# Kernel optimization log

Measured on AMD Instinct MI355X. Metric: run time of the kernel, lower is better.

## Reference

```python
import jax, jax.numpy as jnp
import numpy as np

N = 10000
E = 160000
IN_CH, HID, OUT = 14, 128, 4
HEADS = 8
NEG_SLOPE = 0.2


def setup_inputs() -> dict:
    key = jax.random.key(0)
    ks = jax.random.split(key, 16)
    glorot = lambda k, shape: jax.random.normal(k, shape, jnp.float32) * np.sqrt(2.0 / (shape[0] + shape[-1]))
    inp = {
        'x': jax.random.normal(ks[0], (N, IN_CH), jnp.float32),
        'edge_index': jax.random.randint(ks[1], (2, E), 0, N, jnp.int64),
        # layer 1: 14 -> 8 heads x 128, concat
        'W1': glorot(ks[2], (IN_CH, HEADS * HID)),
        'a_src1': glorot(ks[3], (HEADS, HID)),
        'a_dst1': glorot(ks[4], (HEADS, HID)),
        'b1': jnp.zeros((HEADS * HID,), jnp.float32),
        # layer 2: 1024 -> 8 heads x 128, concat
        'W2': glorot(ks[5], (HEADS * HID, HEADS * HID)),
        'a_src2': glorot(ks[6], (HEADS, HID)),
        'a_dst2': glorot(ks[7], (HEADS, HID)),
        'b2': jnp.zeros((HEADS * HID,), jnp.float32),
        # layer 3: 1024 -> 1 head x 4, mean (concat=False)
        'W3': glorot(ks[8], (HEADS * HID, OUT)),
        'a_src3': glorot(ks[9], (1, OUT)),
        'a_dst3': glorot(ks[10], (1, OUT)),
        'b3': jnp.zeros((OUT,), jnp.float32),
    }
    return inp


def gat_conv(x, src, dst, W, a_src, a_dst, b, heads, out_ch, concat):
    n = x.shape[0]
    h = (x @ W).reshape(n, heads, out_ch)                      # [N,H,C]
    al_s = jnp.sum(h * a_src, axis=-1)                         # [N,H]
    al_d = jnp.sum(h * a_dst, axis=-1)                         # [N,H]
    e = al_s[src] + al_d[dst]                                  # [E,H]
    e = jnp.where(e > 0, e, NEG_SLOPE * e)                     # LeakyReLU(0.2)
    # segment softmax over incoming edges of each dst node
    m = jax.ops.segment_max(e, dst, num_segments=n)
    ex = jnp.exp(e - m[dst])
    z = jax.ops.segment_sum(ex, dst, num_segments=n)
    alpha = ex / (z[dst] + 1e-16)                              # [E,H]
    out = jax.ops.segment_sum(h[src] * alpha[:, :, None], dst, num_segments=n)  # [N,H,C]
    out = out.reshape(n, heads * out_ch) if concat else out.mean(axis=1)
    return out + b


def reference(x, edge_index, W1, a_src1, a_dst1, b1, W2, a_src2, a_dst2, b2, W3, a_src3, a_dst3, b3):
    n = x.shape[0]
    # add self-loops (PyG GATConv default)
    loop = jnp.arange(n, dtype=edge_index.dtype)
    src = jnp.concatenate([edge_index[0], loop])
    dst = jnp.concatenate([edge_index[1], loop])
    # dropout layers are identity in eval mode
    h = gat_conv(x, src, dst, W1, a_src1, a_dst1, b1, HEADS, HID, True)
    h = jax.nn.relu(h)
    h = gat_conv(h, src, dst, W2, a_src2, a_dst2, b2, HEADS, HID, True)
    h = jax.nn.relu(h)
    h = gat_conv(h, src, dst, W3, a_src3, a_dst3, b3, 1, OUT, False)
    h = jax.nn.relu(h)
    return h
```

## Files before the change

### kernel.cpp

```cpp
#include <hip/hip_runtime.h>

typedef unsigned short ushort_t;
typedef unsigned int uint32;

#define N_NODES 10000
#define N_EDGES 160000
#define ET (N_NODES + N_EDGES)
#define MPAD 10112
#define HT 1024
#define HEADS 8
#define NEG 0.2f

#define O_FLAG     0
#define O_SRC      256
#define O_DST      (O_SRC + 680192)
#define O_COUNTS   (O_DST + 680192)
#define O_OFFS     (O_COUNTS + 40192)
#define O_CURS     (O_OFFS + 40192)
#define O_SSORT    (O_CURS + 40192)
#define O_ALS      (O_SSORT + 680192)
#define O_ALD      (O_ALS + 320000)
#define O_AL3S     (O_ALD + 320000)
#define O_AL3D     (O_AL3S + 40192)
#define O_H3       (O_AL3D + 40192)
#define O_XF       (O_H3 + 160000)
#define O_W1F      (O_XF + 560128)
#define O_AS1F     (O_W1F + 57344)
#define O_W3F      (O_AS1F + 24576)
#define O_S3F      (O_W3F + 16384)
#define O_W2T      (O_S3F + 768)
#define O_BUFA     (O_W2T + 2097152)
#define O_BUFB     (O_BUFA + 20709376)

__device__ __forceinline__ float bf2f(ushort_t u){ return __uint_as_float(((uint32)u) << 16); }
__device__ __forceinline__ ushort_t f2bf(float f){
    uint32 x = __float_as_uint(f);
    return (ushort_t)((x + 0x7fffu + ((x >> 16) & 1u)) >> 16);
}
__device__ __forceinline__ void unpack2(uint32 u, float& lo, float& hi){
    lo = __uint_as_float(u << 16);
    hi = __uint_as_float(u & 0xffff0000u);
}

typedef __bf16 bf16x8 __attribute__((ext_vector_type(8)));
typedef float  f32x4  __attribute__((ext_vector_type(4)));

typedef const __attribute__((address_space(1))) uint32* gas1_u32;
typedef       __attribute__((address_space(3))) uint32* las3_u32;

__device__ __forceinline__ void gload_lds16(const void* g, void* l){
    __builtin_amdgcn_global_load_lds((gas1_u32)g, (las3_u32)l, 16, 0, 0);
}

__device__ __forceinline__ int probe_f32(const uint32* __restrict__ w){
    int cnt = 0;
    for (int i = 0; i < 256; i++){
        uint32 e = (w[i] >> 7) & 0xffu;
        cnt += (e >= 64u && e <= 160u) ? 1 : 0;
    }
    return (cnt > 200) ? 0 : 1;
}
__device__ __forceinline__ int probe_edge64(const int* __restrict__ ei){
    int nz = 0;
    for (int i = 0; i < 128; i++) nz |= ei[2*i + 1];
    return (nz == 0) ? 1 : 0;
}

struct CvtArgs {
    const void* src[12];
    float*      dst[12];
    int         n[12];
};

__global__ __launch_bounds__(256) void k_setup(CvtArgs a, const void* __restrict__ W2,
                                               const uint32* __restrict__ w1raw,
                                               const int* __restrict__ eiraw,
                                               int* __restrict__ counts,
                                               ushort_t* __restrict__ W2T,
                                               int* __restrict__ flags){
    __shared__ ushort_t tile[32][33];
    int slice = blockIdx.y;
    int tid = threadIdx.x;
    if (slice < 12){
        int n = a.n[slice];
        int base = blockIdx.x * 1024 + tid * 4;
        if (base >= n) return;
        int f32 = probe_f32(w1raw);
        const void* s = a.src[slice];
        float* d = a.dst[slice];
        #pragma unroll
        for (int j = 0; j < 4; j++){
            int i = base + j;
            if (i < n) d[i] = f32 ? ((const float*)s)[i] : bf2f(((const ushort_t*)s)[i]);
        }
    } else if (slice == 12){
        if (blockIdx.x == 10){
            if (tid == 0) flags[0] = probe_edge64(eiraw);
            if (tid == 1) flags[1] = probe_f32(w1raw);
            return;
        }
        if (blockIdx.x < 10){
            int i0 = blockIdx.x * 1024 + tid * 4;
            if (i0 + 3 < N_NODES){
                *(int4*)(counts + i0) = make_int4(0,0,0,0);
            } else {
                for (int j = 0; j < 4; j++) if (i0 + j < N_NODES) counts[i0 + j] = 0;
            }
        }
    } else {
        int f32 = probe_f32(w1raw);
        int bx = blockIdx.x & 31, by = blockIdx.x >> 5;
        int cx = tid & 31;
        int ry = (tid >> 5) * 4;
        #pragma unroll
        for (int r = 0; r < 4; r++){
            size_t idx = (size_t)(by*32 + ry + r)*1024 + bx*32 + cx;
            tile[ry + r][cx] = f32 ? f2bf(((const float*)W2)[idx]) : ((const ushort_t*)W2)[idx];
        }
        __syncthreads();
        #pragma unroll
        for (int r = 0; r < 4; r++)
            W2T[(size_t)(bx*32 + ry + r)*1024 + by*32 + cx] = tile[cx][ry + r];
    }
}

__global__ __launch_bounds__(256) void k_extract_hist(const void* __restrict__ ei, const int* __restrict__ flags,
                                                      int* __restrict__ src, int* __restrict__ dst,
                                                      int* __restrict__ counts){
    int i = blockIdx.x * 256 + threadIdx.x;
    int is64 = flags[0];
    int s = -1, d = -1;
    if (i < N_EDGES){
        if (is64){
            const long long* p = (const long long*)ei;
            s = (int)p[i]; d = (int)p[N_EDGES + i];
        } else {
            const int* p = (const int*)ei;
            s = p[i]; d = p[N_EDGES + i];
        }
    } else if (i < ET){
        s = i - N_EDGES; d = s;
    }
    if (d >= 0){
        src[i] = s; dst[i] = d;
        atomicAdd(&counts[d], 1);
    }
}

__global__ __launch_bounds__(1024) void k_scan(const int* __restrict__ counts, int* __restrict__ offs,
                                               int* __restrict__ cursors, int n){
    __shared__ int wsum[16];
    __shared__ int running_s;
    int tid = threadIdx.x;
    int lane = tid & 63, wid = tid >> 6;
    if (tid == 0) running_s = 0;
    __syncthreads();
    for (int base = 0; base < n; base += 1024){
        int i = base + tid;
        int v = (i < n) ? counts[i] : 0;
        int x = v;
        #pragma unroll
        for (int d = 1; d < 64; d <<= 1){
            int t = __shfl_up(x, d, 64);
            if (lane >= d) x += t;
        }
        if (lane == 63) wsum[wid] = x;
        __syncthreads();
        if (wid == 0 && lane < 16){
            int w = wsum[lane];
            #pragma unroll
            for (int d = 1; d < 16; d <<= 1){
                int t = __shfl_up(w, d, 64);
                if (lane >= d) w += t;
            }
            wsum[lane] = w;
        }
        __syncthreads();
        int wprefix = (wid == 0) ? 0 : wsum[wid - 1];
        int run = running_s;
        int excl = run + wprefix + (x - v);
        if (i < n){ offs[i] = excl; cursors[i] = excl; }
        __syncthreads();
        if (tid == 0) running_s = run + wsum[15];
        __syncthreads();
    }
    if (tid == 0) offs[n] = running_s;
}

__global__ __launch_bounds__(256) void k_scatter(const int* __restrict__ src, const int* __restrict__ dst,
                                                 int* __restrict__ cursors, int* __restrict__ ssort){
    int i = blockIdx.x * 256 + threadIdx.x;
    if (i < ET){
        int pos = atomicAdd(&cursors[dst[i]], 1);
        ssort[pos] = src[i];
    }
}

__global__ __launch_bounds__(256) void k_gemm1f(const float* __restrict__ x, const float* __restrict__ W1,
                                                const float* __restrict__ a_src, const float* __restrict__ a_dst,
                                                ushort_t* __restrict__ h1,
                                                float* __restrict__ alS, float* __restrict__ alD){
    __shared__ float w1s[14 * HT];
    int tid = threadIdx.x;
    for (int i = tid * 4; i < 14 * HT; i += 1024)
        *(float4*)(w1s + i) = *(const float4*)(W1 + i);
    int c0 = tid * 4;
    float4 sv = *(const float4*)(a_src + c0);
    float4 dv = *(const float4*)(a_dst + c0);
    int head = tid >> 5, l32 = tid & 31;
    __syncthreads();
    for (int n = blockIdx.x; n < N_NODES; n += gridDim.x){
        float a0=0.f, a1=0.f, a2=0.f, a3=0.f;
        #pragma unroll
        for (int k = 0; k < 14; k++){
            float xv = x[n*14 + k];
            float4 w = *(const float4*)(w1s + k*HT + c0);
            a0 += xv*w.x; a1 += xv*w.y; a2 += xv*w.z; a3 += xv*w.w;
        }
        uint2 o;
        o.x = (uint32)f2bf(a0) | ((uint32)f2bf(a1) << 16);
        o.y = (uint32)f2bf(a2) | ((uint32)f2bf(a3) << 16);
        *(uint2*)(h1 + (size_t)n*HT + c0) = o;
        float h0,h1v,h2,h3v;
        unpack2(o.x, h0, h1v); unpack2(o.y, h2, h3v);
        float s = h0*sv.x + h1v*sv.y + h2*sv.z + h3v*sv.w;
        float d = h0*dv.x + h1v*dv.y + h2*dv.z + h3v*dv.w;
        #pragma unroll
        for (int of = 16; of; of >>= 1){ s += __shfl_xor(s, of, 32); d += __shfl_xor(d, of, 32); }
        if (l32 == 0){ alS[n*HEADS + head] = s; alD[n*HEADS + head] = d; }
    }
}

__global__ __launch_bounds__(256) void k_gat_agg(const ushort_t* __restrict__ H, const float* __restrict__ alS,
                                                 const float* __restrict__ alD, const int* __restrict__ offs,
                                                 const int* __restrict__ srcs, const float* __restrict__ bias,
                                                 ushort_t* __restrict__ out){
    int tid = threadIdx.x;
    int wv = tid >> 6, lane = tid & 63;
    int n = blockIdx.x * 2 + (wv >> 1);
    int half = wv & 1;
    int beg = offs[n], end = offs[n+1];
    int head = half*4 + (lane >> 4);
    int slot = lane & 15;
    float ad = alD[n*HEADS + head];

    float m = -1e30f, z = 0.f;
    for (int c = beg; c < end; c += 64){
        int cn = min(64, end - c);
        int sreg = (lane < cn) ? srcs[c + lane] : 0;
        for (int p = slot; p < cn; p += 16){
            int s = __shfl(sreg, p, 64);
            float v = alS[s*HEADS + head] + ad;
            v = v > 0.f ? v : NEG*v;
            if (v > m){ z = z*__expf(m - v) + 1.f; m = v; }
            else z += __expf(v - m);
        }
    }
    #pragma unroll
    for (int o = 1; o < 16; o <<= 1){
        float m2 = __shfl_xor(m, o, 64);
        float z2 = __shfl_xor(z, o, 64);
        float nm = fmaxf(m, m2);
        z = z*__expf(m - nm) + z2*__expf(m2 - nm);
        m = nm;
    }
    float inv = 1.f / (z + 1e-16f);

    int ch0 = half*512 + lane*8;
    const ushort_t* Hc = H + ch0;
    float c0=0.f,c1=0.f,c2=0.f,c3=0.f,c4=0.f,c5=0.f,c6=0.f,c7=0.f;
    for (int c = beg; c < end; c += 64){
        int cn = min(64, end - c);
        int sreg = (lane < cn) ? srcs[c + lane] : 0;
        int j = 0;
        for (; j + 2 <= cn; j += 2){
            int s0 = __shfl(sreg, j, 64);
            int s1 = __shfl(sreg, j+1, 64);
            uint4 u0 = *(const uint4*)(Hc + (size_t)s0*HT);
            uint4 u1 = *(const uint4*)(Hc + (size_t)s1*HT);
            float v0 = alS[s0*HEADS + head] + ad;
            float v1 = alS[s1*HEADS + head] + ad;
            v0 = v0 > 0.f ? v0 : NEG*v0;
            v1 = v1 > 0.f ? v1 : NEG*v1;
            float w0 = __expf(v0 - m) * inv;
            float w1 = __expf(v1 - m) * inv;
            float f0,f1,f2,f3,f4,f5,f6,f7;
            unpack2(u0.x,f0,f1); unpack2(u0.y,f2,f3); unpack2(u0.z,f4,f5); unpack2(u0.w,f6,f7);
            c0+=w0*f0; c1+=w0*f1; c2+=w0*f2; c3+=w0*f3;
            c4+=w0*f4; c5+=w0*f5; c6+=w0*f6; c7+=w0*f7;
            unpack2(u1.x,f0,f1); unpack2(u1.y,f2,f3); unpack2(u1.z,f4,f5); unpack2(u1.w,f6,f7);
            c0+=w1*f0; c1+=w1*f1; c2+=w1*f2; c3+=w1*f3;
            c4+=w1*f4; c5+=w1*f5; c6+=w1*f6; c7+=w1*f7;
        }
        if (j < cn){
            int s0 = __shfl(sreg, j, 64);
            uint4 u0 = *(const uint4*)(Hc + (size_t)s0*HT);
            float v0 = alS[s0*HEADS + head] + ad;
            v0 = v0 > 0.f ? v0 : NEG*v0;
            float w0 = __expf(v0 - m) * inv;
            float f0,f1,f2,f3,f4,f5,f6,f7;
            unpack2(u0.x,f0,f1); unpack2(u0.y,f2,f3); unpack2(u0.z,f4,f5); unpack2(u0.w,f6,f7);
            c0+=w0*f0; c1+=w0*f1; c2+=w0*f2; c3+=w0*f3;
            c4+=w0*f4; c5+=w0*f5; c6+=w0*f6; c7+=w0*f7;
        }
    }
    float4 b0 = *(const float4*)(bias + ch0);
    float4 b1 = *(const float4*)(bias + ch0 + 4);
    c0 = fmaxf(c0+b0.x, 0.f); c1 = fmaxf(c1+b0.y, 0.f);
    c2 = fmaxf(c2+b0.z, 0.f); c3 = fmaxf(c3+b0.w, 0.f);
    c4 = fmaxf(c4+b1.x, 0.f); c5 = fmaxf(c5+b1.y, 0.f);
    c6 = fmaxf(c6+b1.z, 0.f); c7 = fmaxf(c7+b1.w, 0.f);
    uint4 o;
    o.x = (uint32)f2bf(c0) | ((uint32)f2bf(c1) << 16);
    o.y = (uint32)f2bf(c2) | ((uint32)f2bf(c3) << 16);
    o.z = (uint32)f2bf(c4) | ((uint32)f2bf(c5) << 16);
    o.w = (uint32)f2bf(c6) | ((uint32)f2bf(c7) << 16);
    *(uint4*)(out + (size_t)n*HT + ch0) = o;
}

__global__ __launch_bounds__(256) void k_gemm2(const ushort_t* __restrict__ A, const ushort_t* __restrict__ BT,
                                               ushort_t* __restrict__ C,
                                               const float* __restrict__ aS, const float* __restrict__ aD,
                                               float* __restrict__ alS, float* __restrict__ alD){
    __shared__ ushort_t lA[128*32];
    __shared__ ushort_t lB[128*32];
    __shared__ float reds[2][64][2];
    int tid = threadIdx.x;
    int bm = blockIdx.x, bn = blockIdx.y;
    int lane = tid & 63;
    int wave = tid >> 6;
    int wm = (wave & 1) * 64, wn = (wave >> 1) * 64;
    int lm = lane & 15, kg = lane >> 4;
    f32x4 acc[4][4];
    #pragma unroll
    for (int i = 0; i < 4; i++)
        #pragma unroll
        for (int j = 0; j < 4; j++) acc[i][j] = (f32x4)0.0f;

    const int K = 1024;
    int rowA0 = bm * 128, rowB0 = bn * 128;
    for (int k0 = 0; k0 < K; k0 += 32){
        #pragma unroll
        for (int it = 0; it < 2; ++it){
            int s = tid + it*256;
            int r = s >> 2, ks = s & 3;
            gload_lds16(A  + (size_t)(rowA0 + r)*K + k0 + ks*8, lA + s*8);
            gload_lds16(BT + (size_t)(rowB0 + r)*K + k0 + ks*8, lB + s*8);
        }
        __syncthreads();
        bf16x8 af[4], bfr[4];
        #pragma unroll
        for (int mt = 0; mt < 4; mt++) af[mt]  = *(const bf16x8*)(lA + (wm + mt*16 + lm)*32 + kg*8);
        #pragma unroll
        for (int nt = 0; nt < 4; nt++) bfr[nt] = *(const bf16x8*)(lB + (wn + nt*16 + lm)*32 + kg*8);
        #pragma unroll
        for (int mt = 0; mt < 4; mt++)
            #pragma unroll
            for (int nt = 0; nt < 4; nt++)
                acc[mt][nt] = __builtin_amdgcn_mfma_f32_16x16x32_bf16(af[mt], bfr[nt], acc[mt][nt], 0, 0, 0);
        __syncthreads();
    }
    #pragma unroll
    for (int mt = 0; mt < 4; mt++){
        int row_base = bm*128 + wm + mt*16 + kg*4;
        #pragma unroll
        for (int nt = 0; nt < 4; nt++){
            int col = bn*128 + wn + nt*16 + lm;
            #pragma unroll
            for (int r = 0; r < 4; r++){
                int row = row_base + r;
                if (row < N_NODES) C[(size_t)row*HT + col] = f2bf(acc[mt][nt][r]);
            }
        }
    }
    float as_l[4], ad_l[4];
    #pragma unroll
    for (int nt = 0; nt < 4; nt++){
        as_l[nt] = aS[bn*128 + wn + nt*16 + lm];
        ad_l[nt] = aD[bn*128 + wn + nt*16 + lm];
    }
    float psA[4][4], pdA[4][4];
    #pragma unroll
    for (int mt = 0; mt < 4; mt++){
        #pragma unroll
        for (int r = 0; r < 4; r++){
            float ps = acc[mt][0][r]*as_l[0] + acc[mt][1][r]*as_l[1]
                     + acc[mt][2][r]*as_l[2] + acc[mt][3][r]*as_l[3];
            float pd = acc[mt][0][r]*ad_l[0] + acc[mt][1][r]*ad_l[1]
                     + acc[mt][2][r]*ad_l[2] + acc[mt][3][r]*ad_l[3];
            #pragma unroll
            for (int o = 1; o < 16; o <<= 1){ ps += __shfl_xor(ps, o, 64); pd += __shfl_xor(pd, o, 64); }
            psA[mt][r] = ps; pdA[mt][r] = pd;
            if (wn == 64 && lm == 0){
                int rl = mt*16 + kg*4 + r;
                reds[wm >> 6][rl][0] = ps;
                reds[wm >> 6][rl][1] = pd;
            }
        }
    }
    __syncthreads();
    if (wn == 0 && lm == 0){
        #pragma unroll
        for (int mt = 0; mt < 4; mt++){
            #pragma unroll
            for (int r = 0; r < 4; r++){
                int rl = mt*16 + kg*4 + r;
                int row = bm*128 + wm + rl;
                if (row < N_NODES){
                    alS[row*HEADS + bn] = psA[mt][r] + reds[wm >> 6][rl][0];
                    alD[row*HEADS + bn] = pdA[mt][r] + reds[wm >> 6][rl][1];
                }
            }
        }
    }
}

__global__ __launch_bounds__(256) void k_gemm3(const ushort_t* __restrict__ A, const float* __restrict__ W3,
                                               const float* __restrict__ s3,
                                               float* __restrict__ h3, float* __restrict__ al3s, float* __restrict__ al3d){
    int tid = threadIdx.x;
    int lane = tid & 63, wave = tid >> 6;
    int n = blockIdx.x * 4 + wave;
    if (n >= N_NODES) return;
    float4 w3r[16];
    #pragma unroll
    for (int j = 0; j < 16; j++) w3r[j] = ((const float4*)W3)[lane*16 + j];
    const uint4* ap = (const uint4*)(A + (size_t)n*HT + lane*16);
    uint4 u0 = ap[0], u1 = ap[1];
    uint32 uu[8] = {u0.x,u0.y,u0.z,u0.w,u1.x,u1.y,u1.z,u1.w};
    float acc0=0.f, acc1=0.f, acc2=0.f, acc3=0.f;
    #pragma unroll
    for (int p = 0; p < 8; p++){
        float lo, hi;
        unpack2(uu[p], lo, hi);
        float4 wl = w3r[p*2], wh = w3r[p*2+1];
        acc0 += lo*wl.x + hi*wh.x;
        acc1 += lo*wl.y + hi*wh.y;
        acc2 += lo*wl.z + hi*wh.z;
        acc3 += lo*wl.w + hi*wh.w;
    }
    #pragma unroll
    for (int o = 32; o; o >>= 1){
        acc0 += __shfl_xor(acc0, o, 64); acc1 += __shfl_xor(acc1, o, 64);
        acc2 += __shfl_xor(acc2, o, 64); acc3 += __shfl_xor(acc3, o, 64);
    }
    if (lane == 0){
        *(float4*)(h3 + n*4) = make_float4(acc0, acc1, acc2, acc3);
        al3s[n] = acc0*s3[0] + acc1*s3[1] + acc2*s3[2] + acc3*s3[3];
        al3d[n] = acc0*s3[16] + acc1*s3[17] + acc2*s3[18] + acc3*s3[19];
    }
}

__global__ __launch_bounds__(256) void k_gat_agg3(const float* __restrict__ h3, const float* __restrict__ al3s,
                                                  const float* __restrict__ al3d, const int* __restrict__ offs,
                                                  const int* __restrict__ srcs, const float* __restrict__ b3,
                                                  const int* __restrict__ flags, void* __restrict__ out){
    int tid = threadIdx.x;
    int l = tid & 63, wave = tid >> 6;
    int n = blockIdx.x * 4 + wave;
    if (n >= N_NODES) return;
    int beg = offs[n], end = offs[n+1];
    float ad = al3d[n];
    float m = -1e30f;
    for (int e = beg + l; e < end; e += 64){
        float v = al3s[srcs[e]] + ad; v = v > 0.f ? v : NEG*v;
        m = fmaxf(m, v);
    }
    #pragma unroll
    for (int o = 32; o; o >>= 1) m = fmaxf(m, __shfl_xor(m, o, 64));
    float z = 0.f;
    for (int e = beg + l; e < end; e += 64){
        float v = al3s[srcs[e]] + ad; v = v > 0.f ? v : NEG*v;
        z += __expf(v - m);
    }
    #pragma unroll
    for (int o = 32; o; o >>= 1) z += __shfl_xor(z, o, 64);
    float inv = 1.f / (z + 1e-16f);
    float a0=0.f, a1=0.f, a2=0.f, a3=0.f;
    for (int e = beg + l; e < end; e += 64){
        int s = srcs[e];
        float v = al3s[s] + ad; v = v > 0.f ? v : NEG*v;
        float w = __expf(v - m) * inv;
        float4 hv = *(const float4*)(h3 + s*4);
        a0 += w*hv.x; a1 += w*hv.y; a2 += w*hv.z; a3 += w*hv.w;
    }
    #pragma unroll
    for (int o = 32; o; o >>= 1){
        a0 += __shfl_xor(a0, o, 64); a1 += __shfl_xor(a1, o, 64);
        a2 += __shfl_xor(a2, o, 64); a3 += __shfl_xor(a3, o, 64);
    }
    if (l == 0){
        float r0 = fmaxf(a0 + b3[0], 0.f);
        float r1 = fmaxf(a1 + b3[1], 0.f);
        float r2 = fmaxf(a2 + b3[2], 0.f);
        float r3 = fmaxf(a3 + b3[3], 0.f);
        if (flags[1]){
            float* o4 = (float*)out;
            o4[n*4+0]=r0; o4[n*4+1]=r1; o4[n*4+2]=r2; o4[n*4+3]=r3;
        } else {
            ushort_t* o2 = (ushort_t*)out;
            o2[n*4+0]=f2bf(r0); o2[n*4+1]=f2bf(r1); o2[n*4+2]=f2bf(r2); o2[n*4+3]=f2bf(r3);
        }
    }
}

extern "C" void kernel_launch(void* const* d_in, const int* in_sizes, int n_in,
                              void* d_out, int out_size, void* d_ws, size_t ws_size,
                              hipStream_t stream){
    const void* x   = d_in[0];
    const void* ei  = d_in[1];
    const void* W1  = d_in[2];
    const void* as1 = d_in[3];
    const void* ad1 = d_in[4];
    const void* b1  = d_in[5];
    const void* W2  = d_in[6];
    const void* as2 = d_in[7];
    const void* ad2 = d_in[8];
    const void* b2  = d_in[9];
    const void* W3  = d_in[10];
    const void* as3 = d_in[11];
    const void* ad3 = d_in[12];
    const void* b3  = d_in[13];

    char* ws = (char*)d_ws;
    int* flags     = (int*)(ws + O_FLAG);
    int* srcA      = (int*)(ws + O_SRC);
    int* dstA      = (int*)(ws + O_DST);
    int* counts    = (int*)(ws + O_COUNTS);
    int* offs      = (int*)(ws + O_OFFS);
    int* cursors   = (int*)(ws + O_CURS);
    int* ssort     = (int*)(ws + O_SSORT);
    float* alS     = (float*)(ws + O_ALS);
    float* alD     = (float*)(ws + O_ALD);
    float* al3s    = (float*)(ws + O_AL3S);
    float* al3d    = (float*)(ws + O_AL3D);
    float* h3      = (float*)(ws + O_H3);
    float* xF      = (float*)(ws + O_XF);
    float* W1F     = (float*)(ws + O_W1F);
    float* wvecF   = (float*)(ws + O_AS1F);
    float* W3F     = (float*)(ws + O_W3F);
    float* s3F     = (float*)(ws + O_S3F);
    ushort_t* W2T  = (ushort_t*)(ws + O_W2T);
    ushort_t* bufA = (ushort_t*)(ws + O_BUFA);
    ushort_t* bufB = (ushort_t*)(ws + O_BUFB);

    const int EB = (ET + 255) / 256;

    CvtArgs ca;
    ca.src[0]=x;   ca.dst[0]=xF;            ca.n[0]=140000;
    ca.src[1]=W1;  ca.dst[1]=W1F;           ca.n[1]=14336;
    ca.src[2]=as1; ca.dst[2]=wvecF+0*1024;  ca.n[2]=1024;
    ca.src[3]=ad1; ca.dst[3]=wvecF+1*1024;  ca.n[3]=1024;
    ca.src[4]=b1;  ca.dst[4]=wvecF+2*1024;  ca.n[4]=1024;
    ca.src[5]=as2; ca.dst[5]=wvecF+3*1024;  ca.n[5]=1024;
    ca.src[6]=ad2; ca.dst[6]=wvecF+4*1024;  ca.n[6]=1024;
    ca.src[7]=b2;  ca.dst[7]=wvecF+5*1024;  ca.n[7]=1024;
    ca.src[8]=W3;  ca.dst[8]=W3F;           ca.n[8]=4096;
    ca.src[9]=as3; ca.dst[9]=s3F+0;         ca.n[9]=4;
    ca.src[10]=ad3; ca.dst[10]=s3F+16;      ca.n[10]=4;
    ca.src[11]=b3;  ca.dst[11]=s3F+32;      ca.n[11]=4;

    k_setup<<<dim3(1024, 14), 256, 0, stream>>>(ca, W2, (const uint32*)W1, (const int*)ei,
                                                counts, W2T, flags);
    k_extract_hist<<<EB, 256, 0, stream>>>(ei, flags, srcA, dstA, counts);
    k_scan<<<1, 1024, 0, stream>>>(counts, offs, cursors, N_NODES);
    k_scatter<<<EB, 256, 0, stream>>>(srcA, dstA, cursors, ssort);

    k_gemm1f<<<512, 256, 0, stream>>>(xF, W1F, wvecF+0*1024, wvecF+1*1024, bufA, alS, alD);
    k_gat_agg<<<5000, 256, 0, stream>>>(bufA, alS, alD, offs, ssort, wvecF+2*1024, bufB);

    k_gemm2<<<dim3(79, 8), 256, 0, stream>>>(bufB, W2T, bufA, wvecF+3*1024, wvecF+4*1024, alS, alD);
    k_gat_agg<<<5000, 256, 0, stream>>>(bufA, alS, alD, offs, ssort, wvecF+5*1024, bufB);

    k_gemm3<<<2500, 256, 0, stream>>>(bufB, W3F, s3F, h3, al3s, al3d);
    k_gat_agg3<<<2500, 256, 0, stream>>>(h3, al3s, al3d, offs, ssort, s3F+32, flags, d_out);
}
```

Baseline: 339.9 us.

## Unroll aggregation gather by four, swizzle GEMM LDS, remap GEMM blocks per XCD

```diff
diff --git a/kernel.cpp b/kernel.cpp
--- a/kernel.cpp
+++ b/kernel.cpp
@@ -273,17 +273,27 @@
         int cn = min(64, end - c);
         int sreg = (lane < cn) ? srcs[c + lane] : 0;
         int j = 0;
-        for (; j + 2 <= cn; j += 2){
+        for (; j + 4 <= cn; j += 4){
             int s0 = __shfl(sreg, j, 64);
             int s1 = __shfl(sreg, j+1, 64);
+            int s2 = __shfl(sreg, j+2, 64);
+            int s3 = __shfl(sreg, j+3, 64);
+            float e0 = alS[s0*HEADS + head];
+            float e1 = alS[s1*HEADS + head];
+            float e2 = alS[s2*HEADS + head];
+            float e3 = alS[s3*HEADS + head];
             uint4 u0 = *(const uint4*)(Hc + (size_t)s0*HT);
             uint4 u1 = *(const uint4*)(Hc + (size_t)s1*HT);
-            float v0 = alS[s0*HEADS + head] + ad;
-            float v1 = alS[s1*HEADS + head] + ad;
-            v0 = v0 > 0.f ? v0 : NEG*v0;
-            v1 = v1 > 0.f ? v1 : NEG*v1;
+            uint4 u2 = *(const uint4*)(Hc + (size_t)s2*HT);
+            uint4 u3 = *(const uint4*)(Hc + (size_t)s3*HT);
+            float v0 = e0 + ad; v0 = v0 > 0.f ? v0 : NEG*v0;
+            float v1 = e1 + ad; v1 = v1 > 0.f ? v1 : NEG*v1;
+            float v2 = e2 + ad; v2 = v2 > 0.f ? v2 : NEG*v2;
+            float v3 = e3 + ad; v3 = v3 > 0.f ? v3 : NEG*v3;
             float w0 = __expf(v0 - m) * inv;
             float w1 = __expf(v1 - m) * inv;
+            float w2 = __expf(v2 - m) * inv;
+            float w3 = __expf(v3 - m) * inv;
             float f0,f1,f2,f3,f4,f5,f6,f7;
             unpack2(u0.x,f0,f1); unpack2(u0.y,f2,f3); unpack2(u0.z,f4,f5); unpack2(u0.w,f6,f7);
             c0+=w0*f0; c1+=w0*f1; c2+=w0*f2; c3+=w0*f3;
@@ -291,8 +301,14 @@
             unpack2(u1.x,f0,f1); unpack2(u1.y,f2,f3); unpack2(u1.z,f4,f5); unpack2(u1.w,f6,f7);
             c0+=w1*f0; c1+=w1*f1; c2+=w1*f2; c3+=w1*f3;
             c4+=w1*f4; c5+=w1*f5; c6+=w1*f6; c7+=w1*f7;
-        }
-        if (j < cn){
+            unpack2(u2.x,f0,f1); unpack2(u2.y,f2,f3); unpack2(u2.z,f4,f5); unpack2(u2.w,f6,f7);
+            c0+=w2*f0; c1+=w2*f1; c2+=w2*f2; c3+=w2*f3;
+            c4+=w2*f4; c5+=w2*f5; c6+=w2*f6; c7+=w2*f7;
+            unpack2(u3.x,f0,f1); unpack2(u3.y,f2,f3); unpack2(u3.z,f4,f5); unpack2(u3.w,f6,f7);
+            c0+=w3*f0; c1+=w3*f1; c2+=w3*f2; c3+=w3*f3;
+            c4+=w3*f4; c5+=w3*f5; c6+=w3*f6; c7+=w3*f7;
+        }
+        for (; j < cn; j++){
             int s0 = __shfl(sreg, j, 64);
             uint4 u0 = *(const uint4*)(Hc + (size_t)s0*HT);
             float v0 = alS[s0*HEADS + head] + ad;
@@ -325,12 +341,18 @@
     __shared__ ushort_t lA[128*32];
     __shared__ ushort_t lB[128*32];
     __shared__ float reds[2][64][2];
+    int L = blockIdx.x;
+    int xcd = L & 7;
+    int wi  = L >> 3;
+    int bm  = xcd * 10 + (wi >> 3);
+    int bn  = wi & 7;
+    if (bm >= 79) return;
     int tid = threadIdx.x;
-    int bm = blockIdx.x, bn = blockIdx.y;
     int lane = tid & 63;
     int wave = tid >> 6;
     int wm = (wave & 1) * 64, wn = (wave >> 1) * 64;
     int lm = lane & 15, kg = lane >> 4;
+    int sw = (lm >> 1) & 3;
     f32x4 acc[4][4];
     #pragma unroll
     for (int i = 0; i < 4; i++)
@@ -343,16 +365,18 @@
         #pragma unroll
         for (int it = 0; it < 2; ++it){
             int s = tid + it*256;
-            int r = s >> 2, ks = s & 3;
-            gload_lds16(A  + (size_t)(rowA0 + r)*K + k0 + ks*8, lA + s*8);
-            gload_lds16(BT + (size_t)(rowB0 + r)*K + k0 + ks*8, lB + s*8);
+            int r = s >> 2, p = s & 3;
+            int qlog = p ^ ((r >> 1) & 3);
+            gload_lds16(A  + (size_t)(rowA0 + r)*K + k0 + qlog*8, lA + s*8);
+            gload_lds16(BT + (size_t)(rowB0 + r)*K + k0 + qlog*8, lB + s*8);
         }
         __syncthreads();
         bf16x8 af[4], bfr[4];
-        #pragma unroll
-        for (int mt = 0; mt < 4; mt++) af[mt]  = *(const bf16x8*)(lA + (wm + mt*16 + lm)*32 + kg*8);
-        #pragma unroll
-        for (int nt = 0; nt < 4; nt++) bfr[nt] = *(const bf16x8*)(lB + (wn + nt*16 + lm)*32 + kg*8);
+        int kp = (kg ^ sw) * 8;
+        #pragma unroll
+        for (int mt = 0; mt < 4; mt++) af[mt]  = *(const bf16x8*)(lA + (wm + mt*16 + lm)*32 + kp);
+        #pragma unroll
+        for (int nt = 0; nt < 4; nt++) bfr[nt] = *(const bf16x8*)(lB + (wn + nt*16 + lm)*32 + kp);
         #pragma unroll
         for (int mt = 0; mt < 4; mt++)
             #pragma unroll
@@ -569,7 +593,7 @@
     k_gemm1f<<<512, 256, 0, stream>>>(xF, W1F, wvecF+0*1024, wvecF+1*1024, bufA, alS, alD);
     k_gat_agg<<<5000, 256, 0, stream>>>(bufA, alS, alD, offs, ssort, wvecF+2*1024, bufB);
 
-    k_gemm2<<<dim3(79, 8), 256, 0, stream>>>(bufB, W2T, bufA, wvecF+3*1024, wvecF+4*1024, alS, alD);
+    k_gemm2<<<640, 256, 0, stream>>>(bufB, W2T, bufA, wvecF+3*1024, wvecF+4*1024, alS, alD);
     k_gat_agg<<<5000, 256, 0, stream>>>(bufA, alS, alD, offs, ssort, wvecF+5*1024, bufB);
 
     k_gemm3<<<2500, 256, 0, stream>>>(bufB, W3F, s3F, h3, al3s, al3d);
```

After: 330.6 us. 2.7% less time.

## Shrink setup conversions, drop edge staging, retile GEMM2, unroll aggregation gathers

Applied to the files above, without the earlier changes.

```diff
diff --git a/kernel.cpp b/kernel.cpp
--- a/kernel.cpp
+++ b/kernel.cpp
@@ -6,31 +6,27 @@
 #define N_NODES 10000
 #define N_EDGES 160000
 #define ET (N_NODES + N_EDGES)
-#define MPAD 10112
 #define HT 1024
 #define HEADS 8
 #define NEG 0.2f
 
 #define O_FLAG     0
-#define O_SRC      256
-#define O_DST      (O_SRC + 680192)
-#define O_COUNTS   (O_DST + 680192)
+#define O_COUNTS   256
 #define O_OFFS     (O_COUNTS + 40192)
-#define O_CURS     (O_OFFS + 40192)
-#define O_SSORT    (O_CURS + 40192)
-#define O_ALS      (O_SSORT + 680192)
-#define O_ALD      (O_ALS + 320000)
-#define O_AL3S     (O_ALD + 320000)
-#define O_AL3D     (O_AL3S + 40192)
-#define O_H3       (O_AL3D + 40192)
-#define O_XF       (O_H3 + 160000)
-#define O_W1F      (O_XF + 560128)
-#define O_AS1F     (O_W1F + 57344)
-#define O_W3F      (O_AS1F + 24576)
+#define O_SSORT    (O_OFFS + 40192)
+#define O_ALS1     (O_SSORT + 680192)
+#define O_ALD1     (O_ALS1 + 320000)
+#define O_ALS2     (O_ALD1 + 320000)
+#define O_ALD2     (O_ALS2 + 320000)
+#define O_AL3S     O_ALS2
+#define O_AL3D     (O_ALS2 + 40192)
+#define O_H3       (O_ALS2 + 80384)
+#define O_WVEC     (O_ALD2 + 320000)
+#define O_W3F      (O_WVEC + 24576)
 #define O_S3F      (O_W3F + 16384)
 #define O_W2T      (O_S3F + 768)
 #define O_BUFA     (O_W2T + 2097152)
-#define O_BUFB     (O_BUFA + 20709376)
+#define O_BUFB     (O_BUFA + 20480000)
 
 __device__ __forceinline__ float bf2f(ushort_t u){ return __uint_as_float(((uint32)u) << 16); }
 __device__ __forceinline__ ushort_t f2bf(float f){
@@ -60,58 +56,60 @@
     }
     return (cnt > 200) ? 0 : 1;
 }
-__device__ __forceinline__ int probe_edge64(const int* __restrict__ ei){
-    int nz = 0;
-    for (int i = 0; i < 128; i++) nz |= ei[2*i + 1];
-    return (nz == 0) ? 1 : 0;
+__global__ void k_probe(const int* __restrict__ ei, const uint32* __restrict__ w1raw,
+                        int* __restrict__ flags){
+    if (threadIdx.x == 0){
+        int nz = 0;
+        for (int i = 0; i < 128; i++) nz |= ei[2*i + 1];
+        flags[0] = (nz == 0) ? 1 : 0;
+    }
+    if (threadIdx.x == 1) flags[1] = probe_f32(w1raw);
+}
+
+__device__ __forceinline__ float cvt1(const void* p, int i, int f32){
+    return f32 ? ((const float*)p)[i] : bf2f(((const ushort_t*)p)[i]);
 }
 
 struct CvtArgs {
-    const void* src[12];
-    float*      dst[12];
-    int         n[12];
+    const void* vsrc[6];
+    const void* w3src;
+    const void* s3src[3];
 };
 
 __global__ __launch_bounds__(256) void k_setup(CvtArgs a, const void* __restrict__ W2,
-                                               const uint32* __restrict__ w1raw,
-                                               const int* __restrict__ eiraw,
+                                               const int* __restrict__ flags,
+                                               float* __restrict__ wvecF, float* __restrict__ W3F,
+                                               float* __restrict__ s3F,
                                                int* __restrict__ counts,
-                                               ushort_t* __restrict__ W2T,
-                                               int* __restrict__ flags){
+                                               float* __restrict__ alS2, float* __restrict__ alD2,
+                                               ushort_t* __restrict__ W2T){
     __shared__ ushort_t tile[32][33];
-    int slice = blockIdx.y;
-    int tid = threadIdx.x;
-    if (slice < 12){
-        int n = a.n[slice];
-        int base = blockIdx.x * 1024 + tid * 4;
-        if (base >= n) return;
-        int f32 = probe_f32(w1raw);
-        const void* s = a.src[slice];
-        float* d = a.dst[slice];
+    int b = blockIdx.x, tid = threadIdx.x;
+    int f32 = flags[1];
+    if (b < 11){
+        int g = b * 1024 + tid * 4;
         #pragma unroll
         for (int j = 0; j < 4; j++){
-            int i = base + j;
-            if (i < n) d[i] = f32 ? ((const float*)s)[i] : bf2f(((const ushort_t*)s)[i]);
-        }
-    } else if (slice == 12){
-        if (blockIdx.x == 10){
-            if (tid == 0) flags[0] = probe_edge64(eiraw);
-            if (tid == 1) flags[1] = probe_f32(w1raw);
-            return;
-        }
-        if (blockIdx.x < 10){
-            int i0 = blockIdx.x * 1024 + tid * 4;
-            if (i0 + 3 < N_NODES){
-                *(int4*)(counts + i0) = make_int4(0,0,0,0);
-            } else {
-                for (int j = 0; j < 4; j++) if (i0 + j < N_NODES) counts[i0 + j] = 0;
+            int i = g + j;
+            if (i < 6144) wvecF[i] = cvt1(a.vsrc[i >> 10], i & 1023, f32);
+            else if (i < 10240) W3F[i - 6144] = cvt1(a.w3src, i - 6144, f32);
+            else if (i < 10252){
+                int off = i - 10240;
+                s3F[(off >> 2) * 16 + (off & 3)] = cvt1(a.s3src[off >> 2], off & 3, f32);
             }
         }
+    } else if (b < 21){
+        int g = (b - 11) * 1024 + tid * 4;
+        #pragma unroll
+        for (int j = 0; j < 4; j++) if (g + j < N_NODES) counts[g + j] = 0;
+    } else if (b < 178){
+        int g = (b - 21) * 1024 + tid * 4;
+        if (g < 80000){ *(float4*)(alS2 + g) = make_float4(0,0,0,0); }
+        else if (g < 160000){ *(float4*)(alD2 + g - 80000) = make_float4(0,0,0,0); }
     } else {
-        int f32 = probe_f32(w1raw);
-        int bx = blockIdx.x & 31, by = blockIdx.x >> 5;
-        int cx = tid & 31;
-        int ry = (tid >> 5) * 4;
+        int t = b - 178;
+        int bx = t & 31, by = t >> 5;
+        int cx = tid & 31, ry = (tid >> 5) * 4;
         #pragma unroll
         for (int r = 0; r < 4; r++){
             size_t idx = (size_t)(by*32 + ry + r)*1024 + bx*32 + cx;
@@ -125,30 +123,19 @@
 }
 
 __global__ __launch_bounds__(256) void k_extract_hist(const void* __restrict__ ei, const int* __restrict__ flags,
-                                                      int* __restrict__ src, int* __restrict__ dst,
                                                       int* __restrict__ counts){
     int i = blockIdx.x * 256 + threadIdx.x;
     int is64 = flags[0];
-    int s = -1, d = -1;
+    int d = -1;
     if (i < N_EDGES){
-        if (is64){
-            const long long* p = (const long long*)ei;
-            s = (int)p[i]; d = (int)p[N_EDGES + i];
-        } else {
-            const int* p = (const int*)ei;
-            s = p[i]; d = p[N_EDGES + i];
-        }
+        d = is64 ? (int)((const long long*)ei)[N_EDGES + i] : ((const int*)ei)[N_EDGES + i];
     } else if (i < ET){
-        s = i - N_EDGES; d = s;
-    }
-    if (d >= 0){
-        src[i] = s; dst[i] = d;
-        atomicAdd(&counts[d], 1);
-    }
-}
-
-__global__ __launch_bounds__(1024) void k_scan(const int* __restrict__ counts, int* __restrict__ offs,
-                                               int* __restrict__ cursors, int n){
+        d = i - N_EDGES;
+    }
+    if (d >= 0) atomicAdd(&counts[d], 1);
+}
+
+__global__ __launch_bounds__(1024) void k_scan(int* __restrict__ counts, int* __restrict__ offs, int n){
     __shared__ int wsum[16];
     __shared__ int running_s;
     int tid = threadIdx.x;
@@ -179,7 +166,7 @@
         int wprefix = (wid == 0) ? 0 : wsum[wid - 1];
         int run = running_s;
         int excl = run + wprefix + (x - v);
-        if (i < n){ offs[i] = excl; cursors[i] = excl; }
+        if (i < n){ offs[i] = excl; counts[i] = excl; }
         __syncthreads();
         if (tid == 0) running_s = run + wsum[15];
         __syncthreads();
@@ -187,33 +174,54 @@
     if (tid == 0) offs[n] = running_s;
 }
 
-__global__ __launch_bounds__(256) void k_scatter(const int* __restrict__ src, const int* __restrict__ dst,
+__global__ __launch_bounds__(256) void k_scatter(const void* __restrict__ ei, const int* __restrict__ flags,
                                                  int* __restrict__ cursors, int* __restrict__ ssort){
     int i = blockIdx.x * 256 + threadIdx.x;
-    if (i < ET){
-        int pos = atomicAdd(&cursors[dst[i]], 1);
-        ssort[pos] = src[i];
-    }
-}
-
-__global__ __launch_bounds__(256) void k_gemm1f(const float* __restrict__ x, const float* __restrict__ W1,
-                                                const float* __restrict__ a_src, const float* __restrict__ a_dst,
+    if (i >= ET) return;
+    int is64 = flags[0];
+    int s, d;
+    if (i < N_EDGES){
+        if (is64){
+            s = (int)((const long long*)ei)[i];
+            d = (int)((const long long*)ei)[N_EDGES + i];
+        } else {
+            s = ((const int*)ei)[i];
+            d = ((const int*)ei)[N_EDGES + i];
+        }
+    } else { s = i - N_EDGES; d = s; }
+    int pos = atomicAdd(&cursors[d], 1);
+    ssort[pos] = s;
+}
+
+__global__ __launch_bounds__(256) void k_gemm1f(const void* __restrict__ x, const void* __restrict__ W1,
+                                                const int* __restrict__ flags,
+                                                const float* __restrict__ wvecF,
                                                 ushort_t* __restrict__ h1,
                                                 float* __restrict__ alS, float* __restrict__ alD){
     __shared__ float w1s[14 * HT];
     int tid = threadIdx.x;
-    for (int i = tid * 4; i < 14 * HT; i += 1024)
-        *(float4*)(w1s + i) = *(const float4*)(W1 + i);
+    int f32 = flags[1];
+    if (f32){
+        for (int i = tid * 4; i < 14 * HT; i += 1024)
+            *(float4*)(w1s + i) = *(const float4*)((const float*)W1 + i);
+    } else {
+        for (int i = tid * 4; i < 14 * HT; i += 1024){
+            uint2 u = *(const uint2*)((const ushort_t*)W1 + i);
+            unpack2(u.x, w1s[i], w1s[i+1]);
+            unpack2(u.y, w1s[i+2], w1s[i+3]);
+        }
+    }
+    __syncthreads();
     int c0 = tid * 4;
-    float4 sv = *(const float4*)(a_src + c0);
-    float4 dv = *(const float4*)(a_dst + c0);
+    float4 sv = *(const float4*)(wvecF + c0);
+    float4 dv = *(const float4*)(wvecF + 1024 + c0);
     int head = tid >> 5, l32 = tid & 31;
-    __syncthreads();
-    for (int n = blockIdx.x; n < N_NODES; n += gridDim.x){
+    #pragma unroll 1
+    for (int n = blockIdx.x; n < N_NODES; n += 512){
         float a0=0.f, a1=0.f, a2=0.f, a3=0.f;
         #pragma unroll
         for (int k = 0; k < 14; k++){
-            float xv = x[n*14 + k];
+            float xv = f32 ? ((const float*)x)[n*14 + k] : bf2f(((const ushort_t*)x)[n*14 + k]);
             float4 w = *(const float4*)(w1s + k*HT + c0);
             a0 += xv*w.x; a1 += xv*w.y; a2 += xv*w.z; a3 += xv*w.w;
         }
@@ -273,26 +281,28 @@
         int cn = min(64, end - c);
         int sreg = (lane < cn) ? srcs[c + lane] : 0;
         int j = 0;
-        for (; j + 2 <= cn; j += 2){
-            int s0 = __shfl(sreg, j, 64);
-            int s1 = __shfl(sreg, j+1, 64);
-            uint4 u0 = *(const uint4*)(Hc + (size_t)s0*HT);
-            uint4 u1 = *(const uint4*)(Hc + (size_t)s1*HT);
-            float v0 = alS[s0*HEADS + head] + ad;
-            float v1 = alS[s1*HEADS + head] + ad;
-            v0 = v0 > 0.f ? v0 : NEG*v0;
-            v1 = v1 > 0.f ? v1 : NEG*v1;
-            float w0 = __expf(v0 - m) * inv;
-            float w1 = __expf(v1 - m) * inv;
-            float f0,f1,f2,f3,f4,f5,f6,f7;
-            unpack2(u0.x,f0,f1); unpack2(u0.y,f2,f3); unpack2(u0.z,f4,f5); unpack2(u0.w,f6,f7);
-            c0+=w0*f0; c1+=w0*f1; c2+=w0*f2; c3+=w0*f3;
-            c4+=w0*f4; c5+=w0*f5; c6+=w0*f6; c7+=w0*f7;
-            unpack2(u1.x,f0,f1); unpack2(u1.y,f2,f3); unpack2(u1.z,f4,f5); unpack2(u1.w,f6,f7);
-            c0+=w1*f0; c1+=w1*f1; c2+=w1*f2; c3+=w1*f3;
-            c4+=w1*f4; c5+=w1*f5; c6+=w1*f6; c7+=w1*f7;
-        }
-        if (j < cn){
+        for (; j + 8 <= cn; j += 8){
+            int s[8]; uint4 u[8]; float w[8];
+            #pragma unroll
+            for (int q = 0; q < 8; q++) s[q] = __shfl(sreg, j + q, 64);
+            #pragma unroll
+            for (int q = 0; q < 8; q++) u[q] = *(const uint4*)(Hc + (size_t)s[q]*HT);
+            #pragma unroll
+            for (int q = 0; q < 8; q++){
+                float v = alS[s[q]*HEADS + head] + ad;
+                v = v > 0.f ? v : NEG*v;
+                w[q] = __expf(v - m) * inv;
+            }
+            #pragma unroll
+            for (int q = 0; q < 8; q++){
+                float f0,f1,f2,f3,f4,f5,f6,f7;
+                unpack2(u[q].x,f0,f1); unpack2(u[q].y,f2,f3);
+                unpack2(u[q].z,f4,f5); unpack2(u[q].w,f6,f7);
+                c0+=w[q]*f0; c1+=w[q]*f1; c2+=w[q]*f2; c3+=w[q]*f3;
+                c4+=w[q]*f4; c5+=w[q]*f5; c6+=w[q]*f6; c7+=w[q]*f7;
+            }
+        }
+        for (; j < cn; j++){
             int s0 = __shfl(sreg, j, 64);
             uint4 u0 = *(const uint4*)(Hc + (size_t)s0*HT);
             float v0 = alS[s0*HEADS + head] + ad;
@@ -321,51 +331,53 @@
 __global__ __launch_bounds__(256) void k_gemm2(const ushort_t* __restrict__ A, const ushort_t* __restrict__ BT,
                                                ushort_t* __restrict__ C,
                                                const float* __restrict__ aS, const float* __restrict__ aD,
-                                               float* __restrict__ alS, float* __restrict__ alD){
+                                               float* __restrict__ alS2, float* __restrict__ alD2){
     __shared__ ushort_t lA[128*32];
-    __shared__ ushort_t lB[128*32];
-    __shared__ float reds[2][64][2];
+    __shared__ ushort_t lB[64*32];
+    int bn = blockIdx.x, bm = blockIdx.y;
     int tid = threadIdx.x;
-    int bm = blockIdx.x, bn = blockIdx.y;
     int lane = tid & 63;
     int wave = tid >> 6;
-    int wm = (wave & 1) * 64, wn = (wave >> 1) * 64;
+    int wm = wave * 32;
     int lm = lane & 15, kg = lane >> 4;
-    f32x4 acc[4][4];
-    #pragma unroll
-    for (int i = 0; i < 4; i++)
+    f32x4 acc[2][4];
+    #pragma unroll
+    for (int i = 0; i < 2; i++)
         #pragma unroll
         for (int j = 0; j < 4; j++) acc[i][j] = (f32x4)0.0f;
 
-    const int K = 1024;
-    int rowA0 = bm * 128, rowB0 = bn * 128;
-    for (int k0 = 0; k0 < K; k0 += 32){
+    int rowA0 = bm * 128, rowB0 = bn * 64;
+    for (int k0 = 0; k0 < 1024; k0 += 32){
         #pragma unroll
         for (int it = 0; it < 2; ++it){
             int s = tid + it*256;
-            int r = s >> 2, ks = s & 3;
-            gload_lds16(A  + (size_t)(rowA0 + r)*K + k0 + ks*8, lA + s*8);
-            gload_lds16(BT + (size_t)(rowB0 + r)*K + k0 + ks*8, lB + s*8);
-        }
-        __syncthreads();
-        bf16x8 af[4], bfr[4];
-        #pragma unroll
-        for (int mt = 0; mt < 4; mt++) af[mt]  = *(const bf16x8*)(lA + (wm + mt*16 + lm)*32 + kg*8);
-        #pragma unroll
-        for (int nt = 0; nt < 4; nt++) bfr[nt] = *(const bf16x8*)(lB + (wn + nt*16 + lm)*32 + kg*8);
-        #pragma unroll
-        for (int mt = 0; mt < 4; mt++)
+            int r = s >> 2, q = s & 3;
+            int ra = rowA0 + r; if (ra > N_NODES-1) ra = N_NODES-1;
+            gload_lds16(A + (size_t)ra*1024 + k0 + q*8, lA + s*8);
+        }
+        {
+            int r = tid >> 2, q = tid & 3;
+            gload_lds16(BT + (size_t)(rowB0 + r)*1024 + k0 + q*8, lB + tid*8);
+        }
+        __syncthreads();
+        bf16x8 af[2], bfr[4];
+        #pragma unroll
+        for (int mt = 0; mt < 2; mt++) af[mt]  = *(const bf16x8*)(lA + (wm + mt*16 + lm)*32 + kg*8);
+        #pragma unroll
+        for (int nt = 0; nt < 4; nt++) bfr[nt] = *(const bf16x8*)(lB + (nt*16 + lm)*32 + kg*8);
+        #pragma unroll
+        for (int mt = 0; mt < 2; mt++)
             #pragma unroll
             for (int nt = 0; nt < 4; nt++)
                 acc[mt][nt] = __builtin_amdgcn_mfma_f32_16x16x32_bf16(af[mt], bfr[nt], acc[mt][nt], 0, 0, 0);
         __syncthreads();
     }
     #pragma unroll
-    for (int mt = 0; mt < 4; mt++){
+    for (int mt = 0; mt < 2; mt++){
         int row_base = bm*128 + wm + mt*16 + kg*4;
         #pragma unroll
         for (int nt = 0; nt < 4; nt++){
-            int col = bn*128 + wn + nt*16 + lm;
+            int col = bn*64 + nt*16 + lm;
             #pragma unroll
             for (int r = 0; r < 4; r++){
                 int row = row_base + r;
@@ -373,15 +385,15 @@
             }
         }
     }
+    int head = bn >> 1;
     float as_l[4], ad_l[4];
     #pragma unroll
     for (int nt = 0; nt < 4; nt++){
-        as_l[nt] = aS[bn*128 + wn + nt*16 + lm];
-        ad_l[nt] = aD[bn*128 + wn + nt*16 + lm];
-    }
-    float psA[4][4], pdA[4][4];
-    #pragma unroll
-    for (int mt = 0; mt < 4; mt++){
+        as_l[nt] = aS[bn*64 + nt*16 + lm];
+        ad_l[nt] = aD[bn*64 + nt*16 + lm];
+    }
+    #pragma unroll
+    for (int mt = 0; mt < 2; mt++){
         #pragma unroll
         for (int r = 0; r < 4; r++){
             float ps = acc[mt][0][r]*as_l[0] + acc[mt][1][r]*as_l[1]
@@ -390,25 +402,11 @@
                      + acc[mt][2][r]*ad_l[2] + acc[mt][3][r]*ad_l[3];
             #pragma unroll
             for (int o = 1; o < 16; o <<= 1){ ps += __shfl_xor(ps, o, 64); pd += __shfl_xor(pd, o, 64); }
-            psA[mt][r] = ps; pdA[mt][r] = pd;
-            if (wn == 64 && lm == 0){
-                int rl = mt*16 + kg*4 + r;
-                reds[wm >> 6][rl][0] = ps;
-                reds[wm >> 6][rl][1] = pd;
-            }
-        }
-    }
-    __syncthreads();
-    if (wn == 0 && lm == 0){
-        #pragma unroll
-        for (int mt = 0; mt < 4; mt++){
-            #pragma unroll
-            for (int r = 0; r < 4; r++){
-                int rl = mt*16 + kg*4 + r;
-                int row = bm*128 + wm + rl;
+            if (lm == 0){
+                int row = bm*128 + wm + mt*16 + kg*4 + r;
                 if (row < N_NODES){
-                    alS[row*HEADS + bn] = psA[mt][r] + reds[wm >> 6][rl][0];
-                    alD[row*HEADS + bn] = pdA[mt][r] + reds[wm >> 6][rl][1];
+                    atomicAdd(&alS2[row*HEADS + head], ps);
+                    atomicAdd(&alD2[row*HEADS + head], pd);
                 }
             }
         }
@@ -510,34 +508,22 @@
     const void* x   = d_in[0];
     const void* ei  = d_in[1];
     const void* W1  = d_in[2];
-    const void* as1 = d_in[3];
-    const void* ad1 = d_in[4];
-    const void* b1  = d_in[5];
     const void* W2  = d_in[6];
-    const void* as2 = d_in[7];
-    const void* ad2 = d_in[8];
-    const void* b2  = d_in[9];
     const void* W3  = d_in[10];
-    const void* as3 = d_in[11];
-    const void* ad3 = d_in[12];
-    const void* b3  = d_in[13];
 
     char* ws = (char*)d_ws;
     int* flags     = (int*)(ws + O_FLAG);
-    int* srcA      = (int*)(ws + O_SRC);
-    int* dstA      = (int*)(ws + O_DST);
     int* counts    = (int*)(ws + O_COUNTS);
     int* offs      = (int*)(ws + O_OFFS);
-    int* cursors   = (int*)(ws + O_CURS);
     int* ssort     = (int*)(ws + O_SSORT);
-    float* alS     = (float*)(ws + O_ALS);
-    float* alD     = (float*)(ws + O_ALD);
+    float* alS1    = (float*)(ws + O_ALS1);
+    float* alD1    = (float*)(ws + O_ALD1);
+    float* alS2    = (float*)(ws + O_ALS2);
+    float* alD2    = (float*)(ws + O_ALD2);
     float* al3s    = (float*)(ws + O_AL3S);
     float* al3d    = (float*)(ws + O_AL3D);
     float* h3      = (float*)(ws + O_H3);
-    float* xF      = (float*)(ws + O_XF);
-    float* W1F     = (float*)(ws + O_W1F);
-    float* wvecF   = (float*)(ws + O_AS1F);
+    float* wvecF   = (float*)(ws + O_WVEC);
     float* W3F     = (float*)(ws + O_W3F);
     float* s3F     = (float*)(ws + O_S3F);
     ushort_t* W2T  = (ushort_t*)(ws + O_W2T);
@@ -547,31 +533,23 @@
     const int EB = (ET + 255) / 256;
 
     CvtArgs ca;
-    ca.src[0]=x;   ca.dst[0]=xF;            ca.n[0]=140000;
-    ca.src[1]=W1;  ca.dst[1]=W1F;           ca.n[1]=14336;
-    ca.src[2]=as1; ca.dst[2]=wvecF+0*1024;  ca.n[2]=1024;
-    ca.src[3]=ad1; ca.dst[3]=wvecF+1*1024;  ca.n[3]=1024;
-    ca.src[4]=b1;  ca.dst[4]=wvecF+2*1024;  ca.n[4]=1024;
-    ca.src[5]=as2; ca.dst[5]=wvecF+3*1024;  ca.n[5]=1024;
-    ca.src[6]=ad2; ca.dst[6]=wvecF+4*1024;  ca.n[6]=1024;
-    ca.src[7]=b2;  ca.dst[7]=wvecF+5*1024;  ca.n[7]=1024;
-    ca.src[8]=W3;  ca.dst[8]=W3F;           ca.n[8]=4096;
-    ca.src[9]=as3; ca.dst[9]=s3F+0;         ca.n[9]=4;
-    ca.src[10]=ad3; ca.dst[10]=s3F+16;      ca.n[10]=4;
-    ca.src[11]=b3;  ca.dst[11]=s3F+32;      ca.n[11]=4;
-
-    k_setup<<<dim3(1024, 14), 256, 0, stream>>>(ca, W2, (const uint32*)W1, (const int*)ei,
-                                                counts, W2T, flags);
-    k_extract_hist<<<EB, 256, 0, stream>>>(ei, flags, srcA, dstA, counts);
-    k_scan<<<1, 1024, 0, stream>>>(counts, offs, cursors, N_NODES);
-    k_scatter<<<EB, 256, 0, stream>>>(srcA, dstA, cursors, ssort);
-
-    k_gemm1f<<<512, 256, 0, stream>>>(xF, W1F, wvecF+0*1024, wvecF+1*1024, bufA, alS, alD);
-    k_gat_agg<<<5000, 256, 0, stream>>>(bufA, alS, alD, offs, ssort, wvecF+2*1024, bufB);
-
-    k_gemm2<<<dim3(79, 8), 256, 0, stream>>>(bufB, W2T, bufA, wvecF+3*1024, wvecF+4*1024, alS, alD);
-    k_gat_agg<<<5000, 256, 0, stream>>>(bufA, alS, alD, offs, ssort, wvecF+5*1024, bufB);
+    ca.vsrc[0]=d_in[3];  ca.vsrc[1]=d_in[4];  ca.vsrc[2]=d_in[5];
+    ca.vsrc[3]=d_in[7];  ca.vsrc[4]=d_in[8];  ca.vsrc[5]=d_in[9];
+    ca.w3src = W3;
+    ca.s3src[0]=d_in[11]; ca.s3src[1]=d_in[12]; ca.s3src[2]=d_in[13];
+
+    k_probe<<<1, 64, 0, stream>>>((const int*)ei, (const uint32*)W1, flags);
+    k_setup<<<1202, 256, 0, stream>>>(ca, W2, flags, wvecF, W3F, s3F, counts, alS2, alD2, W2T);
+    k_extract_hist<<<EB, 256, 0, stream>>>(ei, flags, counts);
+    k_scan<<<1, 1024, 0, stream>>>(counts, offs, N_NODES);
+    k_scatter<<<EB, 256, 0, stream>>>(ei, flags, counts, ssort);
+
+    k_gemm1f<<<512, 256, 0, stream>>>(x, W1, flags, wvecF, bufA, alS1, alD1);
+    k_gat_agg<<<5000, 256, 0, stream>>>(bufA, alS1, alD1, offs, ssort, wvecF + 2*1024, bufB);
+
+    k_gemm2<<<dim3(16, 79), 256, 0, stream>>>(bufB, W2T, bufA, wvecF + 3*1024, wvecF + 4*1024, alS2, alD2);
+    k_gat_agg<<<5000, 256, 0, stream>>>(bufA, alS2, alD2, offs, ssort, wvecF + 5*1024, bufB);
 
     k_gemm3<<<2500, 256, 0, stream>>>(bufB, W3F, s3F, h3, al3s, al3d);
-    k_gat_agg3<<<2500, 256, 0, stream>>>(h3, al3s, al3d, offs, ssort, s3F+32, flags, d_out);
-}
+    k_gat_agg3<<<2500, 256, 0, stream>>>(h3, al3s, al3d, offs, ssort, s3F + 32, flags, d_out);
+}
```

New measurement: 358.3 us. +5.4%, slower.
